# Optimization experiments

Hardware: AMD Instinct MI355X
Metric: run time of the kernel (lower is better)

## Reference

```python
import jax, jax.numpy as jnp
import numpy as np

K = 512
D = 64


def setup_inputs() -> dict:
    key = jax.random.key(0)
    k1, k2 = jax.random.split(key)
    z_e_x = jax.random.normal(k1, (32, D, 64, 64), dtype=jnp.float32)  # [B, D, H, W]
    # codebook initialized uniform(-1/K, 1/K) as in the torch module
    emb = jax.random.uniform(k2, (K, D), dtype=jnp.float32, minval=-1.0 / K, maxval=1.0 / K)
    return {"z_e_x": z_e_x, "emb": emb}


def reference(z_e_x, emb):
    B, Dc, H, W = z_e_x.shape
    # [B, D, H, W] -> [B*H*W, D]
    z = jnp.transpose(z_e_x, (0, 2, 3, 1)).reshape(-1, Dc)
    z_norm = jnp.sum(z * z, axis=1, keepdims=True)          # [N, 1]
    e_norm = jnp.sum(emb * emb, axis=1)[None, :]            # [1, K]
    dists = z_norm + e_norm - 2.0 * (z @ emb.T)             # [N, K]
    dists = dists.reshape(B, H, W, -1)
    latents = jnp.argmin(dists, axis=-1)                    # [B, H, W] int
    return latents
```

## Files before the change

kernel.cpp:

```cpp
#include <hip/hip_runtime.h>

#define KCODES 512
#define DDIM   64
#define NROWS  131072

typedef short bf16x8 __attribute__((ext_vector_type(8)));
typedef float f32x4  __attribute__((ext_vector_type(4)));
typedef int   i32x4  __attribute__((ext_vector_type(4)));

union frag_cast { i32x4 i; bf16x8 h; };

__device__ __forceinline__ unsigned f32_to_bf16_rne(float x) {
    unsigned u = __float_as_uint(x);
    return (u + 0x7fffu + ((u >> 16) & 1u)) >> 16;
}

__device__ __forceinline__ void gload16(const void* g, void* l) {
    __builtin_amdgcn_global_load_lds(
        (const __attribute__((address_space(1))) void*)g,
        (__attribute__((address_space(3))) void*)l, 16, 0, 0);
}

__global__ __launch_bounds__(64) void k1_prep(const float* __restrict__ emb,
                                              float* __restrict__ en, float* __restrict__ emaxp,
                                              i32x4* __restrict__ efP) {
    const int kt = blockIdx.x, t = threadIdx.x;
    const int krow = t & 15, gq = t >> 4;
    const int k = kt * 16 + krow;

    float er[16];
    float pz = 0.f;
#pragma unroll
    for (int c = 0; c < 2; ++c)
#pragma unroll
        for (int j = 0; j < 8; ++j) {
            float x = emb[k * DDIM + c * 32 + gq * 8 + j];
            er[c * 8 + j] = x;
            pz = fmaf(x, x, pz);
        }

#pragma unroll
    for (int c = 0; c < 2; ++c) {
        unsigned hh[8], hl[8];
#pragma unroll
        for (int j = 0; j < 8; ++j) {
            float x = er[c * 8 + j];
            unsigned h = f32_to_bf16_rne(x);
            float hf = __uint_as_float(h << 16);
            hh[j] = h;
            hl[j] = f32_to_bf16_rne(x - hf);
        }
        i32x4 wh, wl;
#pragma unroll
        for (int i = 0; i < 4; ++i) {
            wh[i] = (int)(hh[2 * i] | (hh[2 * i + 1] << 16));
            wl[i] = (int)(hl[2 * i] | (hl[2 * i + 1] << 16));
        }
        efP[kt * 256 + c * 64 + krow + 16 * gq]       = wh;
        efP[kt * 256 + (2 + c) * 64 + krow + 16 * gq] = wl;
    }

    pz += __shfl_xor(pz, 16);
    pz += __shfl_xor(pz, 32);
    if (t < 16) en[k] = pz;

    float m = pz;
#pragma unroll
    for (int sh = 1; sh <= 8; sh <<= 1) m = fmaxf(m, __shfl_xor(m, sh));
    if (t == 0) emaxp[kt] = m;
}

__global__ __launch_bounds__(512, 8) void k3_fused(
    const float* __restrict__ z, const float* __restrict__ emb,
    const i32x4* __restrict__ efP,
    const float* __restrict__ en_g, const float* __restrict__ emaxp,
    int* __restrict__ out) {

    __shared__ i32x4 sfrag[3][4][64];
    __shared__ float en_l[KCODES];
    __shared__ float zn_l[128];
    __shared__ float zrow_s[8][64];
    __shared__ int   flag_rows[128];
    __shared__ int   nflag;

    const int t = threadIdx.x, blk = blockIdx.x;
    const int n0 = blk * 128;
    const int b = n0 >> 12, hw0 = n0 & 4095;
    const int w = t >> 6, lane = t & 63;
    const int klane = lane & 15, g = lane >> 4;

    if (t == 0) nflag = 0;

    if (w < 4) {
        gload16(efP + 0 * 256 + w * 64 + lane, &sfrag[0][w][0]);
        gload16(efP + 1 * 256 + w * 64 + lane, &sfrag[1][w][0]);
    }

    en_l[t] = (t < KCODES) ? en_g[t] : 0.f;
    if (t < KCODES - 512 + 512) {}

    float em2 = 0.f;
#pragma unroll
    for (int i = 0; i < 32; ++i) em2 = fmaxf(em2, emaxp[i]);
    const float emax = sqrtf(em2) * 1.0001f;

    const float* zbase = z + (size_t)b * (DDIM * 4096) + hw0;
    const int row = w * 16 + klane;
    bf16x8 zh[2], zl[2];
    {
        float zv[16];
#pragma unroll
        for (int c = 0; c < 2; ++c)
#pragma unroll
            for (int j = 0; j < 8; ++j)
                zv[c * 8 + j] = zbase[(size_t)(c * 32 + g * 8 + j) * 4096 + row];
        float pz = 0.f;
#pragma unroll
        for (int c = 0; c < 2; ++c) {
            unsigned hh[8], hl[8];
#pragma unroll
            for (int j = 0; j < 8; ++j) {
                float x = zv[c * 8 + j];
                pz = fmaf(x, x, pz);
                unsigned h = f32_to_bf16_rne(x);
                float hf = __uint_as_float(h << 16);
                hh[j] = h;
                hl[j] = f32_to_bf16_rne(x - hf);
            }
            frag_cast uh, ul;
#pragma unroll
            for (int i = 0; i < 4; ++i) {
                uh.i[i] = (int)(hh[2 * i] | (hh[2 * i + 1] << 16));
                ul.i[i] = (int)(hl[2 * i] | (hl[2 * i + 1] << 16));
            }
            zh[c] = uh.h;
            zl[c] = ul.h;
        }
        pz += __shfl_xor(pz, 16);
        pz += __shfl_xor(pz, 32);
        if (g == 0) zn_l[w * 16 + klane] = pz;
    }
    __syncthreads();

    f32x4 zn4 = *(const f32x4*)&zn_l[w * 16 + g * 4];

    float m1[4], m2[4];
    int i1[4];
#pragma unroll
    for (int r = 0; r < 4; ++r) { m1[r] = 3.4e38f; m2[r] = 3.4e38f; i1[r] = 0; }

    f32x4 zero = {0.f, 0.f, 0.f, 0.f};

    int buf = 0;
#pragma unroll 1
    for (int kt = 0; kt < 32; ++kt) {
        if (kt < 31) { asm volatile("s_waitcnt vmcnt(1)" ::: "memory"); }
        else         { asm volatile("s_waitcnt vmcnt(0)" ::: "memory"); }
        __builtin_amdgcn_s_barrier();
        if (w < 4 && kt + 2 < 32) {
            int ibuf = buf + 2; if (ibuf >= 3) ibuf -= 3;
            gload16(efP + (size_t)(kt + 2) * 256 + w * 64 + lane, &sfrag[ibuf][w][0]);
        }

        frag_cast e0h, e1h, e0l, e1l;
        e0h.i = sfrag[buf][0][lane];
        e1h.i = sfrag[buf][1][lane];
        e0l.i = sfrag[buf][2][lane];
        e1l.i = sfrag[buf][3][lane];
        asm volatile("s_waitcnt lgkmcnt(0)" ::: "memory");
        __builtin_amdgcn_sched_barrier(0);

        const int k = kt * 16 + klane;
        const float enk = en_l[k];
        f32x4 acc = __builtin_amdgcn_mfma_f32_16x16x32_bf16(zh[0], e0h.h, zero, 0, 0, 0);
        acc = __builtin_amdgcn_mfma_f32_16x16x32_bf16(zh[1], e1h.h, acc, 0, 0, 0);
        acc = __builtin_amdgcn_mfma_f32_16x16x32_bf16(zh[0], e0l.h, acc, 0, 0, 0);
        acc = __builtin_amdgcn_mfma_f32_16x16x32_bf16(zh[1], e1l.h, acc, 0, 0, 0);
        acc = __builtin_amdgcn_mfma_f32_16x16x32_bf16(zl[0], e0h.h, acc, 0, 0, 0);
        acc = __builtin_amdgcn_mfma_f32_16x16x32_bf16(zl[1], e1h.h, acc, 0, 0, 0);
#pragma unroll
        for (int r = 0; r < 4; ++r) {
            float d = fmaf(-2.f, acc[r], zn4[r] + enk);
            float o1 = m1[r];
            i1[r] = (d < o1) ? k : i1[r];
            m2[r] = fminf(m2[r], fmaxf(o1, d));
            m1[r] = fminf(o1, d);
        }
        buf = (buf + 1 == 3) ? 0 : buf + 1;
    }

#pragma unroll
    for (int sh = 1; sh <= 8; sh <<= 1) {
#pragma unroll
        for (int r = 0; r < 4; ++r) {
            float om1 = __shfl_xor(m1[r], sh);
            int oi1 = __shfl_xor(i1[r], sh);
            float om2 = __shfl_xor(m2[r], sh);
            float hi = fmaxf(m1[r], om1);
            m2[r] = fminf(fminf(m2[r], om2), hi);
            i1[r] = (om1 < m1[r]) ? oi1 : i1[r];
            m1[r] = fminf(m1[r], om1);
        }
    }

    if (klane == 0) {
        int rowbase = n0 + w * 16 + g * 4;
        i32x4 idx4;
#pragma unroll
        for (int r = 0; r < 4; ++r) idx4[r] = i1[r];
        *(i32x4*)(out + rowbase) = idx4;
#pragma unroll
        for (int r = 0; r < 4; ++r) {
            float zz = zn4[r];
            float W = fmaf(sqrtf(zz) * emax, 1.0e-4f, zz * 1.0e-6f);
            if (m2[r] - m1[r] <= W) {
                int p = atomicAdd(&nflag, 1);
                flag_rows[p] = w * 16 + g * 4 + r;
            }
        }
    }
    __syncthreads();

    const int nf = nflag;
    for (int i = w; i < nf; i += 8) {
        const int lrow = flag_rows[i];
        zrow_s[w][lane] = zbase[(size_t)lane * 4096 + lrow];
        const float znr = zn_l[lrow];
        float best = 3.4e38f;
        int bi = 0;
#pragma unroll 1
        for (int kk = 0; kk < 8; ++kk) {
            int k = lane * 8 + kk;
            const float* e0 = emb + k * DDIM;
            float acc = 0.f;
#pragma unroll
            for (int d = 0; d < DDIM; ++d) acc = fmaf(e0[d], zrow_s[w][d], acc);
            float dist = fmaf(-2.f, acc, znr + en_l[k]);
            if (dist < best) { best = dist; bi = k; }
        }
        unsigned long long key =
            ((unsigned long long)__float_as_uint(best) << 32) | (unsigned)bi;
#pragma unroll
        for (int sh = 32; sh; sh >>= 1) {
            unsigned long long o = __shfl_xor(key, sh);
            key = (o < key) ? o : key;
        }
        if (lane == 0) out[n0 + lrow] = (int)(key & 0xFFFFFFFFull);
    }
}

__global__ void fb_enorm(const float* __restrict__ emb, float* __restrict__ en) {
    int k = blockIdx.x * blockDim.x + threadIdx.x;
    if (k < KCODES) {
        float s = 0.f;
#pragma unroll
        for (int d = 0; d < DDIM; ++d) { float e = emb[k * DDIM + d]; s = fmaf(e, e, s); }
        en[k] = s;
    }
}
__global__ __launch_bounds__(256) void fb_argmin(const float* __restrict__ z,
                                                 const float* __restrict__ emb,
                                                 const float* __restrict__ en,
                                                 int* __restrict__ out, int nrows) {
    int n = blockIdx.x * blockDim.x + threadIdx.x;
    if (n >= nrows) return;
    int b = n >> 12, hw = n & 4095;
    const float* zp = z + (size_t)b * (DDIM * 4096) + hw;
    float zr[DDIM];
#pragma unroll
    for (int d = 0; d < DDIM; ++d) zr[d] = zp[(size_t)d * 4096];
    float zn = 0.f;
#pragma unroll
    for (int d = 0; d < DDIM; ++d) zn = fmaf(zr[d], zr[d], zn);
    float best = 3.4e38f; int bi = 0;
    for (int k0 = 0; k0 < KCODES; k0 += 8) {
        float acc[8];
#pragma unroll
        for (int kk = 0; kk < 8; ++kk) acc[kk] = 0.f;
        const float* e0 = emb + k0 * DDIM;
#pragma unroll
        for (int d = 0; d < DDIM; ++d) {
            float zd = zr[d];
#pragma unroll
            for (int kk = 0; kk < 8; ++kk) acc[kk] = fmaf(e0[kk * DDIM + d], zd, acc[kk]);
        }
#pragma unroll
        for (int kk = 0; kk < 8; ++kk) {
            float dist = fmaf(-2.f, acc[kk], zn + en[k0 + kk]);
            if (dist < best) { best = dist; bi = k0 + kk; }
        }
    }
    out[n] = bi;
}

extern "C" void kernel_launch(void* const* d_in, const int* in_sizes, int n_in,
                              void* d_out, int out_size, void* d_ws, size_t ws_size,
                              hipStream_t stream) {
    const float* z   = (const float*)d_in[0];
    const float* emb = (const float*)d_in[1];
    int* out = (int*)d_out;

    const size_t SZ_EF   = 32 * 4 * 64 * 16;
    const size_t SZ_EN   = KCODES * 4;
    const size_t SZ_EMAX = 128;
    const size_t NEED = SZ_EF + SZ_EN + SZ_EMAX;

    if (ws_size < NEED) {
        float* en = (float*)d_ws;
        fb_enorm<<<2, 256, 0, stream>>>(emb, en);
        fb_argmin<<<NROWS / 256, 256, 0, stream>>>(z, emb, en, out, NROWS);
        return;
    }

    char* p = (char*)d_ws;
    i32x4* efP = (i32x4*)p;   p += SZ_EF;
    float* en  = (float*)p;   p += SZ_EN;
    float* emaxp = (float*)p;

    k1_prep<<<32, 64, 0, stream>>>(emb, en, emaxp, efP);
    k3_fused<<<NROWS / 128, 512, 0, stream>>>(z, emb, efP, en, emaxp, out);
}
```

Baseline: 96.30 us.

## Give each wave two row tiles, load codebook in larger double-buffered chunks

Each block now has 4 waves instead of 8, and each wave handles two 16-row tiles, so every codebook fragment read from LDS feeds twice as many MFMAs. The codebook streams in 8-tile chunks with double buffering, which cuts barriers from 32 to 4 per block. Dropping zn from the per-element distance is valid because zn is constant per row and does not change the argmin. Manual bf16 rounding is replaced by the packed v_cvt_pk_bf16_f32 instruction. The cost is more registers per thread and fewer waves per block, which may reduce latency hiding.

```diff
diff --git a/kernel.cpp b/kernel.cpp
--- a/kernel.cpp
+++ b/kernel.cpp
@@ -10,9 +10,17 @@
 
 union frag_cast { i32x4 i; bf16x8 h; };
 
-__device__ __forceinline__ unsigned f32_to_bf16_rne(float x) {
-    unsigned u = __float_as_uint(x);
-    return (u + 0x7fffu + ((u >> 16) & 1u)) >> 16;
+__device__ __forceinline__ unsigned cvt_pk_bf16(float x0, float x1) {
+    unsigned r;
+    asm volatile("v_cvt_pk_bf16_f32 %0, %1, %2" : "=v"(r) : "v"(x0), "v"(x1));
+    return r;
+}
+
+__device__ __forceinline__ void split_pair(float x0, float x1, unsigned& h, unsigned& l) {
+    h = cvt_pk_bf16(x0, x1);
+    float hf0 = __uint_as_float(h << 16);
+    float hf1 = __uint_as_float(h & 0xffff0000u);
+    l = cvt_pk_bf16(x0 - hf0, x1 - hf1);
 }
 
 __device__ __forceinline__ void gload16(const void* g, void* l) {
@@ -41,20 +49,13 @@
 
 #pragma unroll
     for (int c = 0; c < 2; ++c) {
-        unsigned hh[8], hl[8];
-#pragma unroll
-        for (int j = 0; j < 8; ++j) {
-            float x = er[c * 8 + j];
-            unsigned h = f32_to_bf16_rne(x);
-            float hf = __uint_as_float(h << 16);
-            hh[j] = h;
-            hl[j] = f32_to_bf16_rne(x - hf);
-        }
         i32x4 wh, wl;
 #pragma unroll
         for (int i = 0; i < 4; ++i) {
-            wh[i] = (int)(hh[2 * i] | (hh[2 * i + 1] << 16));
-            wl[i] = (int)(hl[2 * i] | (hl[2 * i + 1] << 16));
+            unsigned h, l;
+            split_pair(er[c * 8 + 2 * i], er[c * 8 + 2 * i + 1], h, l);
+            wh[i] = (int)h;
+            wl[i] = (int)l;
         }
         efP[kt * 256 + c * 64 + krow + 16 * gq]       = wh;
         efP[kt * 256 + (2 + c) * 64 + krow + 16 * gq] = wl;
@@ -70,16 +71,16 @@
     if (t == 0) emaxp[kt] = m;
 }
 
-__global__ __launch_bounds__(512, 8) void k3_fused(
+__global__ __launch_bounds__(256, 4) void k3_fused(
     const float* __restrict__ z, const float* __restrict__ emb,
     const i32x4* __restrict__ efP,
     const float* __restrict__ en_g, const float* __restrict__ emaxp,
     int* __restrict__ out) {
 
-    __shared__ i32x4 sfrag[3][4][64];
+    __shared__ i32x4 sfrag[2][8][4][64];
     __shared__ float en_l[KCODES];
     __shared__ float zn_l[128];
-    __shared__ float zrow_s[8][64];
+    __shared__ float zrow_s[4][64];
     __shared__ int   flag_rows[128];
     __shared__ int   nflag;
 
@@ -91,13 +92,19 @@
 
     if (t == 0) nflag = 0;
 
-    if (w < 4) {
-        gload16(efP + 0 * 256 + w * 64 + lane, &sfrag[0][w][0]);
-        gload16(efP + 1 * 256 + w * 64 + lane, &sfrag[1][w][0]);
-    }
-
-    en_l[t] = (t < KCODES) ? en_g[t] : 0.f;
-    if (t < KCODES - 512 + 512) {}
+    auto issue_chunk = [&](int kg, int bsel) {
+        const i32x4* src = efP + (size_t)kg * 2048;
+        i32x4* dst = &sfrag[bsel][0][0][0];
+#pragma unroll
+        for (int i = 0; i < 8; ++i) {
+            int q = w * 8 + i;
+            gload16(src + q * 64 + lane, dst + q * 64);
+        }
+    };
+    issue_chunk(0, 0);
+
+    en_l[t] = en_g[t];
+    en_l[t + 256] = en_g[t + 256];
 
     float em2 = 0.f;
 #pragma unroll
@@ -105,9 +112,10 @@
     const float emax = sqrtf(em2) * 1.0001f;
 
     const float* zbase = z + (size_t)b * (DDIM * 4096) + hw0;
-    const int row = w * 16 + klane;
-    bf16x8 zh[2], zl[2];
-    {
+    bf16x8 zh[2][2], zl[2][2];
+#pragma unroll
+    for (int tl = 0; tl < 2; ++tl) {
+        const int row = w * 32 + tl * 16 + klane;
         float zv[16];
 #pragma unroll
         for (int c = 0; c < 2; ++c)
@@ -117,112 +125,108 @@
         float pz = 0.f;
 #pragma unroll
         for (int c = 0; c < 2; ++c) {
-            unsigned hh[8], hl[8];
-#pragma unroll
-            for (int j = 0; j < 8; ++j) {
-                float x = zv[c * 8 + j];
-                pz = fmaf(x, x, pz);
-                unsigned h = f32_to_bf16_rne(x);
-                float hf = __uint_as_float(h << 16);
-                hh[j] = h;
-                hl[j] = f32_to_bf16_rne(x - hf);
+            frag_cast uh, ul;
+#pragma unroll
+            for (int i = 0; i < 4; ++i) {
+                float x0 = zv[c * 8 + 2 * i], x1 = zv[c * 8 + 2 * i + 1];
+                pz = fmaf(x0, x0, pz);
+                pz = fmaf(x1, x1, pz);
+                unsigned h, l;
+                split_pair(x0, x1, h, l);
+                uh.i[i] = (int)h;
+                ul.i[i] = (int)l;
             }
-            frag_cast uh, ul;
-#pragma unroll
-            for (int i = 0; i < 4; ++i) {
-                uh.i[i] = (int)(hh[2 * i] | (hh[2 * i + 1] << 16));
-                ul.i[i] = (int)(hl[2 * i] | (hl[2 * i + 1] << 16));
-            }
-            zh[c] = uh.h;
-            zl[c] = ul.h;
+            zh[tl][c] = uh.h;
+            zl[tl][c] = ul.h;
         }
         pz += __shfl_xor(pz, 16);
         pz += __shfl_xor(pz, 32);
-        if (g == 0) zn_l[w * 16 + klane] = pz;
+        if (g == 0) zn_l[w * 32 + tl * 16 + klane] = pz;
+    }
+
+    float m1[2][4], m2[2][4];
+    int i1[2][4];
+#pragma unroll
+    for (int tl = 0; tl < 2; ++tl)
+#pragma unroll
+        for (int r = 0; r < 4; ++r) { m1[tl][r] = 3.4e38f; m2[tl][r] = 3.4e38f; i1[tl][r] = 0; }
+
+    f32x4 zero = {0.f, 0.f, 0.f, 0.f};
+
+#pragma unroll 1
+    for (int kg = 0; kg < 4; ++kg) {
+        asm volatile("s_waitcnt vmcnt(0)" ::: "memory");
+        __builtin_amdgcn_s_barrier();
+        if (kg + 1 < 4) issue_chunk(kg + 1, (kg + 1) & 1);
+        const int bsel = kg & 1;
+#pragma unroll 2
+        for (int ktl = 0; ktl < 8; ++ktl) {
+            const int k = (kg * 8 + ktl) * 16 + klane;
+            const float enk = en_l[k];
+            frag_cast e0h, e1h, e0l, e1l;
+            e0h.i = sfrag[bsel][ktl][0][lane];
+            e1h.i = sfrag[bsel][ktl][1][lane];
+            e0l.i = sfrag[bsel][ktl][2][lane];
+            e1l.i = sfrag[bsel][ktl][3][lane];
+#pragma unroll
+            for (int tl = 0; tl < 2; ++tl) {
+                f32x4 acc = __builtin_amdgcn_mfma_f32_16x16x32_bf16(zh[tl][0], e0h.h, zero, 0, 0, 0);
+                acc = __builtin_amdgcn_mfma_f32_16x16x32_bf16(zh[tl][1], e1h.h, acc, 0, 0, 0);
+                acc = __builtin_amdgcn_mfma_f32_16x16x32_bf16(zh[tl][0], e0l.h, acc, 0, 0, 0);
+                acc = __builtin_amdgcn_mfma_f32_16x16x32_bf16(zh[tl][1], e1l.h, acc, 0, 0, 0);
+                acc = __builtin_amdgcn_mfma_f32_16x16x32_bf16(zl[tl][0], e0h.h, acc, 0, 0, 0);
+                acc = __builtin_amdgcn_mfma_f32_16x16x32_bf16(zl[tl][1], e1h.h, acc, 0, 0, 0);
+#pragma unroll
+                for (int r = 0; r < 4; ++r) {
+                    float d = fmaf(-2.f, acc[r], enk);
+                    float o1 = m1[tl][r];
+                    i1[tl][r] = (d < o1) ? k : i1[tl][r];
+                    m2[tl][r] = fminf(m2[tl][r], fmaxf(o1, d));
+                    m1[tl][r] = fminf(o1, d);
+                }
+            }
+        }
+    }
+
+#pragma unroll
+    for (int sh = 1; sh <= 8; sh <<= 1) {
+#pragma unroll
+        for (int tl = 0; tl < 2; ++tl)
+#pragma unroll
+            for (int r = 0; r < 4; ++r) {
+                float om1 = __shfl_xor(m1[tl][r], sh);
+                int oi1 = __shfl_xor(i1[tl][r], sh);
+                float om2 = __shfl_xor(m2[tl][r], sh);
+                float hi = fmaxf(m1[tl][r], om1);
+                m2[tl][r] = fminf(fminf(m2[tl][r], om2), hi);
+                i1[tl][r] = (om1 < m1[tl][r]) ? oi1 : i1[tl][r];
+                m1[tl][r] = fminf(m1[tl][r], om1);
+            }
+    }
+
+    if (klane == 0) {
+#pragma unroll
+        for (int tl = 0; tl < 2; ++tl) {
+            int rowbase = n0 + w * 32 + tl * 16 + g * 4;
+            i32x4 idx4;
+#pragma unroll
+            for (int r = 0; r < 4; ++r) idx4[r] = i1[tl][r];
+            *(i32x4*)(out + rowbase) = idx4;
+#pragma unroll
+            for (int r = 0; r < 4; ++r) {
+                float zz = zn_l[w * 32 + tl * 16 + g * 4 + r];
+                float W = fmaf(sqrtf(zz) * emax, 1.0e-4f, zz * 1.0e-6f);
+                if (m2[tl][r] - m1[tl][r] <= W) {
+                    int p = atomicAdd(&nflag, 1);
+                    flag_rows[p] = w * 32 + tl * 16 + g * 4 + r;
+                }
+            }
+        }
     }
     __syncthreads();
 
-    f32x4 zn4 = *(const f32x4*)&zn_l[w * 16 + g * 4];
-
-    float m1[4], m2[4];
-    int i1[4];
-#pragma unroll
-    for (int r = 0; r < 4; ++r) { m1[r] = 3.4e38f; m2[r] = 3.4e38f; i1[r] = 0; }
-
-    f32x4 zero = {0.f, 0.f, 0.f, 0.f};
-
-    int buf = 0;
-#pragma unroll 1
-    for (int kt = 0; kt < 32; ++kt) {
-        if (kt < 31) { asm volatile("s_waitcnt vmcnt(1)" ::: "memory"); }
-        else         { asm volatile("s_waitcnt vmcnt(0)" ::: "memory"); }
-        __builtin_amdgcn_s_barrier();
-        if (w < 4 && kt + 2 < 32) {
-            int ibuf = buf + 2; if (ibuf >= 3) ibuf -= 3;
-            gload16(efP + (size_t)(kt + 2) * 256 + w * 64 + lane, &sfrag[ibuf][w][0]);
-        }
-
-        frag_cast e0h, e1h, e0l, e1l;
-        e0h.i = sfrag[buf][0][lane];
-        e1h.i = sfrag[buf][1][lane];
-        e0l.i = sfrag[buf][2][lane];
-        e1l.i = sfrag[buf][3][lane];
-        asm volatile("s_waitcnt lgkmcnt(0)" ::: "memory");
-        __builtin_amdgcn_sched_barrier(0);
-
-        const int k = kt * 16 + klane;
-        const float enk = en_l[k];
-        f32x4 acc = __builtin_amdgcn_mfma_f32_16x16x32_bf16(zh[0], e0h.h, zero, 0, 0, 0);
-        acc = __builtin_amdgcn_mfma_f32_16x16x32_bf16(zh[1], e1h.h, acc, 0, 0, 0);
-        acc = __builtin_amdgcn_mfma_f32_16x16x32_bf16(zh[0], e0l.h, acc, 0, 0, 0);
-        acc = __builtin_amdgcn_mfma_f32_16x16x32_bf16(zh[1], e1l.h, acc, 0, 0, 0);
-        acc = __builtin_amdgcn_mfma_f32_16x16x32_bf16(zl[0], e0h.h, acc, 0, 0, 0);
-        acc = __builtin_amdgcn_mfma_f32_16x16x32_bf16(zl[1], e1h.h, acc, 0, 0, 0);
-#pragma unroll
-        for (int r = 0; r < 4; ++r) {
-            float d = fmaf(-2.f, acc[r], zn4[r] + enk);
-            float o1 = m1[r];
-            i1[r] = (d < o1) ? k : i1[r];
-            m2[r] = fminf(m2[r], fmaxf(o1, d));
-            m1[r] = fminf(o1, d);
-        }
-        buf = (buf + 1 == 3) ? 0 : buf + 1;
-    }
-
-#pragma unroll
-    for (int sh = 1; sh <= 8; sh <<= 1) {
-#pragma unroll
-        for (int r = 0; r < 4; ++r) {
-            float om1 = __shfl_xor(m1[r], sh);
-            int oi1 = __shfl_xor(i1[r], sh);
-            float om2 = __shfl_xor(m2[r], sh);
-            float hi = fmaxf(m1[r], om1);
-            m2[r] = fminf(fminf(m2[r], om2), hi);
-            i1[r] = (om1 < m1[r]) ? oi1 : i1[r];
-            m1[r] = fminf(m1[r], om1);
-        }
-    }
-
-    if (klane == 0) {
-        int rowbase = n0 + w * 16 + g * 4;
-        i32x4 idx4;
-#pragma unroll
-        for (int r = 0; r < 4; ++r) idx4[r] = i1[r];
-        *(i32x4*)(out + rowbase) = idx4;
-#pragma unroll
-        for (int r = 0; r < 4; ++r) {
-            float zz = zn4[r];
-            float W = fmaf(sqrtf(zz) * emax, 1.0e-4f, zz * 1.0e-6f);
-            if (m2[r] - m1[r] <= W) {
-                int p = atomicAdd(&nflag, 1);
-                flag_rows[p] = w * 16 + g * 4 + r;
-            }
-        }
-    }
-    __syncthreads();
-
     const int nf = nflag;
-    for (int i = w; i < nf; i += 8) {
+    for (int i = w; i < nf; i += 4) {
         const int lrow = flag_rows[i];
         zrow_s[w][lane] = zbase[(size_t)lane * 4096 + lrow];
         const float znr = zn_l[lrow];
@@ -318,5 +322,5 @@
     float* emaxp = (float*)p;
 
     k1_prep<<<32, 64, 0, stream>>>(emb, en, emaxp, efP);
-    k3_fused<<<NROWS / 128, 512, 0, stream>>>(z, emb, efP, en, emaxp, out);
-}
+    k3_fused<<<NROWS / 128, 256, 0, stream>>>(z, emb, efP, en, emaxp, out);
+}
```

Result: faster. 82.30 us (-14.5%).
